# Performance work log

Hardware: AMD Instinct MI355X
Metric: run time of the kernel (lower is better)

## Reference

```python
import jax, jax.numpy as jnp
import numpy as np

EPS = 1e-8  # torch cosine_similarity norm clamp
TEMP = 1.0

def _gelu(h):
    return jax.nn.gelu(h, approximate=False)  # torch nn.GELU default (erf)

def _layernorm(h, g, b, eps=1e-5):
    mu = jnp.mean(h, axis=-1, keepdims=True)
    var = jnp.var(h, axis=-1, keepdims=True)
    return (h - mu) * jax.lax.rsqrt(var + eps) * g + b

def _encoder(h, eW1, eb1, eW2, eb2, eW3, eb3, ln_g, ln_b):
    h = _gelu(h @ eW1 + eb1)
    h = _gelu(h @ eW2 + eb2)
    h = h @ eW3 + eb3
    return _layernorm(h, ln_g, ln_b)

def _normalize(v):
    n = jnp.sqrt(jnp.sum(v * v, axis=-1, keepdims=True))
    return v / jnp.maximum(n, EPS)

def setup_inputs() -> dict:
    key = jax.random.key(0)
    ks = jax.random.split(key, 8)
    B, D, H, K = 16384, 512, 512, 11
    s = 0.02
    return {
        'x': jax.random.normal(ks[0], (B, D), jnp.float32),
        'tW1': jax.random.normal(ks[1], (K, D, H), jnp.float32) * s,
        'tb1': jnp.zeros((K, H), jnp.float32),
        'tW2': jax.random.normal(ks[2], (K, H, H), jnp.float32) * s,
        'tb2': jnp.zeros((K, H), jnp.float32),
        'tW3': jax.random.normal(ks[3], (K, H, D), jnp.float32) * s,
        'tb3': jnp.zeros((K, D), jnp.float32),
        'eW1': jax.random.normal(ks[4], (D, H), jnp.float32) * s,
        'eb1': jnp.zeros((H,), jnp.float32),
        'eW2': jax.random.normal(ks[5], (H, H), jnp.float32) * s,
        'eb2': jnp.zeros((H,), jnp.float32),
        'eW3': jax.random.normal(ks[6], (H, H), jnp.float32) * s,
        'eb3': jnp.zeros((H,), jnp.float32),
        'ln_g': jnp.ones((H,), jnp.float32),
        'ln_b': jnp.zeros((H,), jnp.float32),
    }

def reference(x, tW1, tb1, tW2, tb2, tW3, tb3, eW1, eb1, eW2, eb2, eW3, eb3, ln_g, ln_b):
    K = tW1.shape[0]
    # K learned transforms, vectorized over k: [K, B, D]
    h = _gelu(jnp.einsum('bi,kij->kbj', x, tW1) + tb1[:, None, :])
    h = _gelu(jnp.einsum('kbi,kij->kbj', h, tW2) + tb2[:, None, :])
    tx = jnp.einsum('kbi,kij->kbj', h, tW3) + tb3[:, None, :]
    # shared encoder on x and on each transformed view
    z = _encoder(x, eW1, eb1, eW2, eb2, eW3, eb3, ln_g, ln_b)      # [B, H]
    zk = _encoder(tx, eW1, eb1, eW2, eb2, eW3, eb3, ln_g, ln_b)    # [K, B, H]
    zn = _normalize(z)
    zkn = _normalize(zk)
    pos = jnp.einsum('bh,kbh->kb', zn, zkn) / TEMP                 # sim(z, z_k)
    S = jnp.einsum('lbh,kbh->lkb', zkn, zkn) / TEMP                # sim(z_l, z_k)
    diag = jnp.eye(K, dtype=bool)[:, :, None]
    Sm = jnp.where(diag, -jnp.inf, S)                              # drop l == k
    all_terms = jnp.concatenate([pos[None], Sm], axis=0)           # [K+1, K, B]
    log_den = jax.nn.logsumexp(all_terms, axis=0)                  # [K, B]
    return -jnp.sum(pos - log_den, axis=0)                         # [B]
```

## Files before the change

### kernel.cpp

```cpp
#include <hip/hip_runtime.h>
#include <hip/hip_bf16.h>
#include <cstdint>

typedef __attribute__((ext_vector_type(8))) short short8;
typedef __attribute__((ext_vector_type(4))) float f32x4;
typedef __attribute__((ext_vector_type(4))) short short4v;

__device__ __forceinline__ float b2f(short s) {
    unsigned u = ((unsigned)(unsigned short)s) << 16;
    return __builtin_bit_cast(float, u);
}
__device__ __forceinline__ short f2b(float f) {
    unsigned u = __builtin_bit_cast(unsigned, f);
    u += 0x7fff + ((u >> 16) & 1);
    return (short)(u >> 16);
}

__device__ __forceinline__ float gelu_t(float x) {
    const float c1 = 2.302184829f;
    const float c2 = 0.102947246f;
    float x2 = x * x;
    float t  = __builtin_fmaf(c2, x2, c1);
    float e  = __builtin_amdgcn_exp2f(x * t);
    return x - __fdividef(x, e + 1.0f);
}

__device__ __forceinline__ void async16(const void* g, void* l) {
    __builtin_amdgcn_global_load_lds(
        (const __attribute__((address_space(1))) unsigned int*)g,
        (__attribute__((address_space(3))) unsigned int*)l, 16, 0, 0);
}

#define VMW(N) asm volatile("s_waitcnt vmcnt(" #N ")" ::: "memory")

template<bool GELU>
__global__ __launch_bounds__(512)
void gemm_bt(const short* __restrict__ A, long sA,
             const short* __restrict__ Bt, long sB,
             const float* __restrict__ bias, long sBias,
             short* __restrict__ C, long sC) {
    const int z = blockIdx.z;
    A    += (long)z * sA;
    Bt   += (long)z * sB;
    bias += (long)z * sBias;
    C    += (long)z * sC;

    const int nwg = (int)gridDim.x;
    const int bx  = (int)blockIdx.x;
    int flat = bx;
    if ((nwg & 7) == 0) { const int q = nwg >> 3; flat = (bx & 7) * q + (bx >> 3); }
    const long arow0 = (long)(flat >> 1) * 256;
    const long brow0 = (long)(flat & 1) * 256;

    __shared__ alignas(16) short smem[2 * 32768];

    const int tid  = threadIdx.x;
    const int lane = tid & 63;
    const int w    = tid >> 6;
    const int wrow = w >> 2, wcol = w & 3;
    const int lr = lane & 15, hi = lane >> 4;

    f32x4 acc[8][4] = {};

    auto stageH = [&](int st, int sks, int sB_) {
        short* reg = smem + (st & 1) * 32768 + (sB_ ? 16384 : 0) + sks * 8192;
        const short* srcb = sB_ ? Bt : A;
        const long r0g = sB_ ? brow0 : arow0;
        const int kc = st * 64 + sks * 32;
#pragma unroll
        for (int jj = 0; jj < 2; ++jj) {
            const int R = w * 32 + jj * 16;
            const int row = R + (lane >> 2);
            const int gc = (lane & 3) ^ ((row >> 1) & 3);
            async16(srcb + (r0g + row) * 512 + kc + gc * 8, reg + R * 32);
        }
    };

    stageH(0, 0, 0); stageH(0, 0, 1);
    stageH(0, 1, 0); stageH(0, 1, 1);
    stageH(1, 0, 0); stageH(1, 0, 1);

    short8 b[4];

#pragma unroll
    for (int i = 0; i < 4; ++i) {
#pragma unroll
        for (int p = 0; p < 8; ++p) {
            const int tau = 2 * i + (p >> 2);
            const int ks  = (p >> 1) & 1;
            const int mh  = p & 1;
            const short* Ar = smem + (tau & 1) * 32768 + ks * 8192;
            const short* Br = Ar + 16384;

            if (mh == 0) {
                if (i < 3)       { VMW(8); }
                else if (p == 0) { VMW(8); }
                else if (p == 2) { VMW(8); }
                else if (p == 4) { VMW(4); }
                else             { VMW(0); }
                __builtin_amdgcn_s_barrier();
                __builtin_amdgcn_sched_barrier(0);
#pragma unroll
                for (int n = 0; n < 4; ++n) {
                    const int row = wcol * 64 + n * 16 + lr;
                    b[n] = *(const short8*)&Br[row * 32 + ((hi ^ ((row >> 1) & 3)) << 3)];
                }
            }

            short8 a[4];
#pragma unroll
            for (int j = 0; j < 4; ++j) {
                const int row = wrow * 128 + (mh * 4 + j) * 16 + lr;
                a[j] = *(const short8*)&Ar[row * 32 + ((hi ^ ((row >> 1) & 3)) << 3)];
            }

            {
                const int st  = (p < 2) ? 2 * i + 1 : (p < 6) ? 2 * i + 2 : 2 * i + 3;
                const int sks = (p < 2) ? 1 : (p < 4) ? 0 : (p < 6) ? 1 : 0;
                const int sB_ = p & 1;
                if (st < 8) stageH(st, sks, sB_);
            }

            __builtin_amdgcn_s_setprio(1);
#pragma unroll
            for (int j = 0; j < 4; ++j)
#pragma unroll
                for (int n = 0; n < 4; ++n)
                    acc[mh * 4 + j][n] = __builtin_amdgcn_mfma_f32_16x16x32_bf16(
                        a[j], b[n], acc[mh * 4 + j][n], 0, 0, 0);
            __builtin_amdgcn_s_setprio(0);

            if (mh == 1) {
                __builtin_amdgcn_sched_barrier(0);
                __builtin_amdgcn_s_barrier();
            }
        }
    }

    short* E = smem + w * (32 * 72);
    const int cl = lr, rl = hi * 4;
#pragma unroll
    for (int h = 0; h < 4; ++h) {
#pragma unroll
        for (int n = 0; n < 4; ++n) {
            const int col = (int)brow0 + wcol * 64 + n * 16 + cl;
            const float bs = bias[col];
            const int ecol = n * 16 + cl;
#pragma unroll
            for (int ml = 0; ml < 2; ++ml) {
                const int m = h * 2 + ml;
                float g0 = acc[m][n][0] + bs, g1 = acc[m][n][1] + bs;
                float g2 = acc[m][n][2] + bs, g3 = acc[m][n][3] + bs;
                if (GELU) { g0 = gelu_t(g0); g1 = gelu_t(g1); g2 = gelu_t(g2); g3 = gelu_t(g3); }
                unsigned p01, p23;
                asm("v_cvt_pk_bf16_f32 %0, %1, %2" : "=v"(p01) : "v"(g0), "v"(g1));
                asm("v_cvt_pk_bf16_f32 %0, %1, %2" : "=v"(p23) : "v"(g2), "v"(g3));
                const int r0 = ml * 16 + rl;
                E[(r0 + 0) * 72 + ecol] = (short)(p01 & 0xffff);
                E[(r0 + 1) * 72 + ecol] = (short)(p01 >> 16);
                E[(r0 + 2) * 72 + ecol] = (short)(p23 & 0xffff);
                E[(r0 + 3) * 72 + ecol] = (short)(p23 >> 16);
            }
        }
#pragma unroll
        for (int chunk = 0; chunk < 4; ++chunk) {
            const int rloc = chunk * 8 + (lane >> 3);
            const int c0   = (lane & 7) * 8;
            short8 v = *(const short8*)&E[rloc * 72 + c0];
            *(short8*)&C[(arow0 + wrow * 128 + h * 32 + rloc) * 512
                         + brow0 + wcol * 64 + c0] = v;
        }
    }
}

__global__ __launch_bounds__(256)
void transpose_conv(const float* __restrict__ src, short* __restrict__ dst) {
    __shared__ float t[32][33];
    const long moff = (long)blockIdx.z * 512 * 512;
    const float* s = src + moff;
    short* d = dst + moff;
    const int tx = threadIdx.x & 31, ty = threadIdx.x >> 5;
    const int bi = blockIdx.x, bj = blockIdx.y;
#pragma unroll
    for (int j = 0; j < 4; ++j)
        t[ty + j * 8][tx] = s[(long)(bi * 32 + ty + j * 8) * 512 + bj * 32 + tx];
    __syncthreads();
#pragma unroll
    for (int j = 0; j < 4; ++j)
        d[(long)(bj * 32 + ty + j * 8) * 512 + bi * 32 + tx] = f2b(t[tx][ty + j * 8]);
}

__global__ __launch_bounds__(256)
void conv_f32_bf16(const float* __restrict__ src, short* __restrict__ dst, long n) {
    long i = ((long)blockIdx.x * 256 + threadIdx.x) * 4;
    if (i >= n) return;
    float4 f = *(const float4*)&src[i];
    short4v o;
    o[0] = f2b(f.x); o[1] = f2b(f.y); o[2] = f2b(f.z); o[3] = f2b(f.w);
    *(short4v*)&dst[i] = o;
}

__global__ __launch_bounds__(256)
void bias_fold(const float* __restrict__ tb3, const short* __restrict__ wtE1,
               const float* __restrict__ eb1, float* __restrict__ bB) {
    const int wid = threadIdx.x >> 6, lane = threadIdx.x & 63;
    const int idx = blockIdx.x * 4 + wid;
    const int k = idx >> 9, n = idx & 511;
    short8 wv = *(const short8*)&wtE1[(long)n * 512 + lane * 8];
    const float* tb = tb3 + (long)k * 512 + lane * 8;
    float s = 0.f;
#pragma unroll
    for (int j = 0; j < 8; ++j) s += b2f(wv[j]) * tb[j];
#pragma unroll
    for (int o = 1; o < 64; o <<= 1) s += __shfl_xor(s, o, 64);
    if (lane == 0) bB[(long)(k + 1) * 512 + n] = s + eb1[n];
}

__global__ __launch_bounds__(256)
void ln_loss(const short* __restrict__ H, const float* __restrict__ g,
             const float* __restrict__ bta, float* __restrict__ out, int CH) {
    __shared__ alignas(16) short Z[4][16 * 520];
    const int wid = threadIdx.x >> 6, lane = threadIdx.x & 63;
    const long b = (long)blockIdx.x * 4 + wid;
    short* Zw = &Z[wid][0];

#pragma unroll
    for (int r = 12; r < 16; ++r)
        *(short8*)&Zw[r * 520 + lane * 8] = (short8){0, 0, 0, 0, 0, 0, 0, 0};

    for (int s = 0; s < 12; ++s) {
        short8 t = *(const short8*)&H[((long)s * CH + b) * 512 + lane * 8];
        float v[8];
        float sum = 0.f, ss = 0.f;
#pragma unroll
        for (int j = 0; j < 8; ++j) { v[j] = b2f(t[j]); sum += v[j]; ss += v[j] * v[j]; }
#pragma unroll
        for (int o = 1; o < 64; o <<= 1) { sum += __shfl_xor(sum, o, 64); ss += __shfl_xor(ss, o, 64); }
        const float mu = sum * (1.f / 512.f);
        const float rs = rsqrtf(ss * (1.f / 512.f) - mu * mu + 1e-5f);
        float y[8]; float nsq = 0.f;
#pragma unroll
        for (int j = 0; j < 8; ++j) {
            const int col = lane * 8 + j;
            y[j] = (v[j] - mu) * rs * g[col] + bta[col];
            nsq += y[j] * y[j];
        }
#pragma unroll
        for (int o = 1; o < 64; o <<= 1) nsq += __shfl_xor(nsq, o, 64);
        const float inv = 1.f / fmaxf(sqrtf(nsq), 1e-8f);
        short8 o8;
#pragma unroll
        for (int j = 0; j < 8; ++j) o8[j] = f2b(y[j] * inv);
        *(short8*)&Zw[s * 520 + lane * 8] = o8;
    }

    f32x4 acc = {0.f, 0.f, 0.f, 0.f};
    const int lr = lane & 15, hi = lane >> 4;
#pragma unroll
    for (int st = 0; st < 16; ++st) {
        short8 a = *(const short8*)&Zw[lr * 520 + st * 32 + hi * 8];
        acc = __builtin_amdgcn_mfma_f32_16x16x32_bf16(a, a, acc, 0, 0, 0);
    }
    const int col = lr;
    float lmax = -3.0e38f;
    bool valid[4];
#pragma unroll
    for (int i = 0; i < 4; ++i) {
        const int row = hi * 4 + i;
        valid[i] = (row < 12) && (row != col);
        if (valid[i]) lmax = fmaxf(lmax, acc[i]);
    }
    lmax = fmaxf(lmax, __shfl_xor(lmax, 16, 64));
    lmax = fmaxf(lmax, __shfl_xor(lmax, 32, 64));
    float esum = 0.f;
#pragma unroll
    for (int i = 0; i < 4; ++i)
        if (valid[i]) esum += __builtin_amdgcn_exp2f((acc[i] - lmax) * 1.44269504f);
    esum += __shfl_xor(esum, 16, 64);
    esum += __shfl_xor(esum, 32, 64);
    float contrib = 0.f;
    if (hi == 0 && col >= 1 && col <= 11) {
        const float logden = lmax + __builtin_amdgcn_logf(esum) * 0.6931471806f;
        contrib = acc[0] - logden;
    }
#pragma unroll
    for (int o = 1; o < 16; o <<= 1) contrib += __shfl_xor(contrib, o, 64);
    if (lane == 0) out[b] = -contrib;
}

extern "C" void kernel_launch(void* const* d_in, const int* in_sizes, int n_in,
                              void* d_out, int out_size, void* d_ws, size_t ws_size,
                              hipStream_t stream) {
    const float* x    = (const float*)d_in[0];
    const float* tW1  = (const float*)d_in[1];
    const float* tb1  = (const float*)d_in[2];
    const float* tW2  = (const float*)d_in[3];
    const float* tb2  = (const float*)d_in[4];
    const float* tW3  = (const float*)d_in[5];
    const float* tb3  = (const float*)d_in[6];
    const float* eW1  = (const float*)d_in[7];
    const float* eb1  = (const float*)d_in[8];
    const float* eW2  = (const float*)d_in[9];
    const float* eb2  = (const float*)d_in[10];
    const float* eW3  = (const float*)d_in[11];
    const float* eb3  = (const float*)d_in[12];
    const float* ln_g = (const float*)d_in[13];
    const float* ln_b = (const float*)d_in[14];

    const int  B    = in_sizes[0] / 512;
    const long WMAT = 512L * 512L;

    int  c  = 1;
    long CH = B;
    for (;;) {
        CH = (long)B / c;
        size_t need = (size_t)48 * WMAT * 2 + (512 + 12 * 512) * 4
                    + (size_t)24 * CH * 512 * 2 + 8192;
        if (need <= ws_size || CH <= 256) break;
        c <<= 1;
    }
    const long SLAB = 12L * CH * 512;

    short* wt   = (short*)d_ws;
    short* Mt   = wt + 36L * WMAT;
    float* zero512 = (float*)(Mt + 12L * WMAT);
    float* bB   = zero512 + 512;
    short* S    = (short*)(bB + 12 * 512);
    short* T    = S + SLAB;

    {
        dim3 tgK(16, 16, 11), tg1(16, 16, 1);
        transpose_conv<<<tgK, 256, 0, stream>>>(tW1, wt + 0L * WMAT);
        transpose_conv<<<tgK, 256, 0, stream>>>(tW2, wt + 11L * WMAT);
        conv_f32_bf16<<<(unsigned)((11 * WMAT / 4 + 255) / 256), 256, 0, stream>>>(
            tW3, wt + 22L * WMAT, 11 * WMAT);
        transpose_conv<<<tg1, 256, 0, stream>>>(eW1, wt + 33L * WMAT);
        transpose_conv<<<tg1, 256, 0, stream>>>(eW2, wt + 34L * WMAT);
        transpose_conv<<<tg1, 256, 0, stream>>>(eW3, wt + 35L * WMAT);

        hipMemsetAsync(zero512, 0, 512 * sizeof(float), stream);
        gemm_bt<false><<<dim3(4, 1, 11), 512, 0, stream>>>(
            wt + 33L * WMAT, 0, wt + 22L * WMAT, WMAT, zero512, 0, Mt + WMAT, WMAT);
        hipMemcpyAsync(Mt, wt + 33L * WMAT, WMAT * sizeof(short),
                       hipMemcpyDeviceToDevice, stream);
        hipMemcpyAsync(bB, eb1, 512 * sizeof(float),
                       hipMemcpyDeviceToDevice, stream);
        bias_fold<<<(11 * 512) / 4, 256, 0, stream>>>(tb3, wt + 33L * WMAT, eb1, bB);
    }

    const long SC = CH * 512;
    const dim3 gT((unsigned)(CH / 256 * 2), 1, 11);
    const dim3 gF((unsigned)(CH / 256 * 2), 1, 12);
    const dim3 gE((unsigned)(12 * CH / 256 * 2), 1, 1);

    for (int ch = 0; ch < c; ++ch) {
        conv_f32_bf16<<<(unsigned)((SC / 4 + 255) / 256), 256, 0, stream>>>(
            x + (long)ch * SC, S, SC);

        gemm_bt<true ><<<gT, 512, 0, stream>>>(S, 0,  wt + 0L * WMAT,  WMAT, tb1, 512, T + SC, SC);
        gemm_bt<true ><<<gT, 512, 0, stream>>>(T + SC, SC, wt + 11L * WMAT, WMAT, tb2, 512, S + SC, SC);
        gemm_bt<true ><<<gF, 512, 0, stream>>>(S, SC, Mt, WMAT, bB, 512, T, SC);
        gemm_bt<true ><<<gE, 512, 0, stream>>>(T, 0, wt + 34L * WMAT, 0, eb2, 0, S, 0);
        gemm_bt<false><<<gE, 512, 0, stream>>>(S, 0, wt + 35L * WMAT, 0, eb3, 0, T, 0);

        ln_loss<<<(unsigned)(CH / 4), 256, 0, stream>>>(
            T, ln_g, ln_b, (float*)d_out + (long)ch * CH, (int)CH);
    }
}
```

Before: 962.0 us.

## Fuse the per-view MLP and encoder GEMM chain into one persistent-tile kernel

Replaces the five separate batched GEMM launches with a single kernel in which each workgroup keeps a 64-row activation tile resident in LDS. It streams each layer's weights through double-buffered LDS, applies bias and GELU in place, and writes only the final encoder output. This removes the global round-trips of intermediate activations and shrinks the workspace. The risks are the much smaller M tile (64 rows against 256 before), which lowers MFMA reuse of weights and raises weight traffic. The 64KB activation tile plus weight buffers may also limit occupancy.

```diff
diff --git a/kernel.cpp b/kernel.cpp
--- a/kernel.cpp
+++ b/kernel.cpp
@@ -5,6 +5,8 @@
 typedef __attribute__((ext_vector_type(8))) short short8;
 typedef __attribute__((ext_vector_type(4))) float f32x4;
 typedef __attribute__((ext_vector_type(4))) short short4v;
+
+#define WM 262144L
 
 __device__ __forceinline__ float b2f(short s) {
     unsigned u = ((unsigned)(unsigned short)s) << 16;
@@ -32,6 +34,132 @@
 }
 
 #define VMW(N) asm volatile("s_waitcnt vmcnt(" #N ")" ::: "memory")
+
+__global__ __launch_bounds__(512)
+void mega(const short* __restrict__ xb, const short* __restrict__ wt,
+          const short* __restrict__ Mt,
+          const float* __restrict__ tb1, const float* __restrict__ tb2,
+          const float* __restrict__ bB,
+          const float* __restrict__ eb2v, const float* __restrict__ eb3v,
+          short* __restrict__ T, int CH) {
+    __shared__ alignas(16) short Ash[64 * 512];
+    __shared__ alignas(16) short Wb[2][512 * 32];
+
+    const int tid = threadIdx.x, lane = tid & 63, w = tid >> 6;
+    const int lr = lane & 15, hi = lane >> 4;
+    const int kview = blockIdx.z;
+    const long row0 = (long)blockIdx.x * 64;
+    const int L  = (kview == 0) ? 3 : 5;
+    const int NS = L * 16;
+
+#pragma unroll
+    for (int it = 0; it < 8; ++it) {
+        const int idx = it * 512 + tid;
+        const int r = idx >> 6, cch = idx & 63;
+        short8 v = *(const short8*)&xb[(row0 + r) * 512 + cch * 8];
+        *(short8*)&Ash[r * 512 + ((cch ^ (r & 15)) << 3)] = v;
+    }
+    asm volatile("s_waitcnt lgkmcnt(0)" ::: "memory");
+
+    auto wmat = [&](int l) -> const short* {
+        if (kview == 0) return (l == 0) ? Mt : (l == 1) ? wt + 34 * WM : wt + 35 * WM;
+        return (l == 0) ? wt + (long)(kview - 1) * WM
+             : (l == 1) ? wt + (long)(11 + kview - 1) * WM
+             : (l == 2) ? Mt + (long)kview * WM
+             : (l == 3) ? wt + 34 * WM : wt + 35 * WM;
+    };
+
+    auto stageW = [&](int q, int s) {
+        const short* Wsrc = wmat(s >> 4);
+        const int kc = (s & 15) * 32;
+        short* dst = &Wb[q][0];
+#pragma unroll
+        for (int i = 0; i < 4; ++i) {
+            const int R = w * 64 + i * 16;
+            const int row = R + (lane >> 2);
+            const int gc = (lane & 3) ^ ((row >> 1) & 3);
+            async16(Wsrc + (long)row * 512 + kc + gc * 8, dst + R * 32);
+        }
+    };
+
+    f32x4 acc[4][4] = {};
+    stageW(0, 0);
+    int buf = 0;
+    for (int s = 0; s < NS; ++s) {
+        if (s + 1 < NS) { stageW(buf ^ 1, s + 1); VMW(4); }
+        else            { VMW(0); }
+        __builtin_amdgcn_sched_barrier(0);
+        __builtin_amdgcn_s_barrier();
+        __builtin_amdgcn_sched_barrier(0);
+
+        const short* Wc = &Wb[buf][0];
+        short8 a[4], b[4];
+        const int ach = (s & 15) * 4 + hi;
+#pragma unroll
+        for (int n = 0; n < 4; ++n) {
+            const int nr = w * 64 + n * 16 + lr;
+            b[n] = *(const short8*)&Wc[nr * 32 + ((hi ^ ((nr >> 1) & 3)) << 3)];
+        }
+#pragma unroll
+        for (int m = 0; m < 4; ++m) {
+            const int row = m * 16 + lr;
+            a[m] = *(const short8*)&Ash[row * 512 + ((ach ^ (row & 15)) << 3)];
+        }
+        __builtin_amdgcn_s_setprio(1);
+#pragma unroll
+        for (int m = 0; m < 4; ++m)
+#pragma unroll
+            for (int n = 0; n < 4; ++n)
+                acc[m][n] = __builtin_amdgcn_mfma_f32_16x16x32_bf16(
+                    a[m], b[n], acc[m][n], 0, 0, 0);
+        __builtin_amdgcn_s_setprio(0);
+
+        __builtin_amdgcn_sched_barrier(0);
+        __builtin_amdgcn_s_barrier();
+
+        if ((s & 15) == 15) {
+            const int l = s >> 4;
+            const float* bp; bool g;
+            if (kview == 0) {
+                bp = (l == 0) ? bB : (l == 1) ? eb2v : eb3v; g = (l < 2);
+            } else {
+                bp = (l == 0) ? tb1 + (long)(kview - 1) * 512
+                   : (l == 1) ? tb2 + (long)(kview - 1) * 512
+                   : (l == 2) ? bB + (long)kview * 512
+                   : (l == 3) ? eb2v : eb3v;
+                g = (l < 4);
+            }
+#pragma unroll
+            for (int n = 0; n < 4; ++n) {
+                const int col = w * 64 + n * 16 + lr;
+                const float bv = bp[col];
+#pragma unroll
+                for (int m = 0; m < 4; ++m) {
+#pragma unroll
+                    for (int i = 0; i < 4; ++i) {
+                        const int row = m * 16 + hi * 4 + i;
+                        float v = acc[m][n][i] + bv;
+                        if (g) v = gelu_t(v);
+                        Ash[row * 512 + (((col >> 3) ^ (row & 15)) << 3) + (col & 7)] = f2b(v);
+                    }
+                    acc[m][n] = (f32x4){0.f, 0.f, 0.f, 0.f};
+                }
+            }
+            asm volatile("s_waitcnt lgkmcnt(0)" ::: "memory");
+        }
+        buf ^= 1;
+    }
+
+    __builtin_amdgcn_s_barrier();
+
+#pragma unroll
+    for (int it = 0; it < 8; ++it) {
+        const int idx = it * 512 + tid;
+        const int r = idx >> 6, cch = idx & 63;
+        short8 v = *(const short8*)&Ash[r * 512 + ((cch ^ (r & 15)) << 3)];
+        *(short8*)&T[((long)kview * CH + row0 + r) * 512 + cch * 8] = v;
+    }
+}
 
 template<bool GELU>
 __global__ __launch_bounds__(512)
@@ -81,7 +209,6 @@
     stageH(1, 0, 0); stageH(1, 0, 1);
 
     short8 b[4];
-
 #pragma unroll
     for (int i = 0; i < 4; ++i) {
 #pragma unroll
@@ -113,14 +240,12 @@
                 const int row = wrow * 128 + (mh * 4 + j) * 16 + lr;
                 a[j] = *(const short8*)&Ar[row * 32 + ((hi ^ ((row >> 1) & 3)) << 3)];
             }
-
             {
                 const int st  = (p < 2) ? 2 * i + 1 : (p < 6) ? 2 * i + 2 : 2 * i + 3;
                 const int sks = (p < 2) ? 1 : (p < 4) ? 0 : (p < 6) ? 1 : 0;
                 const int sB_ = p & 1;
                 if (st < 8) stageH(st, sks, sB_);
             }
-
             __builtin_amdgcn_s_setprio(1);
 #pragma unroll
             for (int j = 0; j < 4; ++j)
@@ -307,61 +432,53 @@
     const float* ln_g = (const float*)d_in[13];
     const float* ln_b = (const float*)d_in[14];
 
-    const int  B    = in_sizes[0] / 512;
-    const long WMAT = 512L * 512L;
+    const int  B = in_sizes[0] / 512;
 
     int  c  = 1;
     long CH = B;
     for (;;) {
         CH = (long)B / c;
-        size_t need = (size_t)48 * WMAT * 2 + (512 + 12 * 512) * 4
-                    + (size_t)24 * CH * 512 * 2 + 8192;
+        size_t need = (size_t)48 * WM * 2 + (512 + 12 * 512) * 4
+                    + (size_t)13 * CH * 512 * 2 + 8192;
         if (need <= ws_size || CH <= 256) break;
         c <<= 1;
     }
-    const long SLAB = 12L * CH * 512;
 
     short* wt   = (short*)d_ws;
-    short* Mt   = wt + 36L * WMAT;
-    float* zero512 = (float*)(Mt + 12L * WMAT);
+    short* Mt   = wt + 36L * WM;
+    float* zero512 = (float*)(Mt + 12L * WM);
     float* bB   = zero512 + 512;
-    short* S    = (short*)(bB + 12 * 512);
-    short* T    = S + SLAB;
+    short* xb   = (short*)(bB + 12 * 512);
+    short* T    = xb + CH * 512;
 
     {
         dim3 tgK(16, 16, 11), tg1(16, 16, 1);
-        transpose_conv<<<tgK, 256, 0, stream>>>(tW1, wt + 0L * WMAT);
-        transpose_conv<<<tgK, 256, 0, stream>>>(tW2, wt + 11L * WMAT);
-        conv_f32_bf16<<<(unsigned)((11 * WMAT / 4 + 255) / 256), 256, 0, stream>>>(
-            tW3, wt + 22L * WMAT, 11 * WMAT);
-        transpose_conv<<<tg1, 256, 0, stream>>>(eW1, wt + 33L * WMAT);
-        transpose_conv<<<tg1, 256, 0, stream>>>(eW2, wt + 34L * WMAT);
-        transpose_conv<<<tg1, 256, 0, stream>>>(eW3, wt + 35L * WMAT);
+        transpose_conv<<<tgK, 256, 0, stream>>>(tW1, wt + 0L * WM);
+        transpose_conv<<<tgK, 256, 0, stream>>>(tW2, wt + 11L * WM);
+        conv_f32_bf16<<<(unsigned)((11 * WM / 4 + 255) / 256), 256, 0, stream>>>(
+            tW3, wt + 22L * WM, 11 * WM);
+        transpose_conv<<<tg1, 256, 0, stream>>>(eW1, wt + 33L * WM);
+        transpose_conv<<<tg1, 256, 0, stream>>>(eW2, wt + 34L * WM);
+        transpose_conv<<<tg1, 256, 0, stream>>>(eW3, wt + 35L * WM);
 
         hipMemsetAsync(zero512, 0, 512 * sizeof(float), stream);
         gemm_bt<false><<<dim3(4, 1, 11), 512, 0, stream>>>(
-            wt + 33L * WMAT, 0, wt + 22L * WMAT, WMAT, zero512, 0, Mt + WMAT, WMAT);
-        hipMemcpyAsync(Mt, wt + 33L * WMAT, WMAT * sizeof(short),
+            wt + 33L * WM, 0, wt + 22L * WM, WM, zero512, 0, Mt + WM, WM);
+        hipMemcpyAsync(Mt, wt + 33L * WM, WM * sizeof(short),
                        hipMemcpyDeviceToDevice, stream);
         hipMemcpyAsync(bB, eb1, 512 * sizeof(float),
                        hipMemcpyDeviceToDevice, stream);
-        bias_fold<<<(11 * 512) / 4, 256, 0, stream>>>(tb3, wt + 33L * WMAT, eb1, bB);
+        bias_fold<<<(11 * 512) / 4, 256, 0, stream>>>(tb3, wt + 33L * WM, eb1, bB);
     }
 
     const long SC = CH * 512;
-    const dim3 gT((unsigned)(CH / 256 * 2), 1, 11);
-    const dim3 gF((unsigned)(CH / 256 * 2), 1, 12);
-    const dim3 gE((unsigned)(12 * CH / 256 * 2), 1, 1);
+    const dim3 gM((unsigned)(CH / 64), 1, 12);
 
     for (int ch = 0; ch < c; ++ch) {
         conv_f32_bf16<<<(unsigned)((SC / 4 + 255) / 256), 256, 0, stream>>>(
-            x + (long)ch * SC, S, SC);
-
-        gemm_bt<true ><<<gT, 512, 0, stream>>>(S, 0,  wt + 0L * WMAT,  WMAT, tb1, 512, T + SC, SC);
-        gemm_bt<true ><<<gT, 512, 0, stream>>>(T + SC, SC, wt + 11L * WMAT, WMAT, tb2, 512, S + SC, SC);
-        gemm_bt<true ><<<gF, 512, 0, stream>>>(S, SC, Mt, WMAT, bB, 512, T, SC);
-        gemm_bt<true ><<<gE, 512, 0, stream>>>(T, 0, wt + 34L * WMAT, 0, eb2, 0, S, 0);
-        gemm_bt<false><<<gE, 512, 0, stream>>>(S, 0, wt + 35L * WMAT, 0, eb3, 0, T, 0);
+            x + (long)ch * SC, xb, SC);
+
+        mega<<<gM, 512, 0, stream>>>(xb, wt, Mt, tb1, tb2, bB, eb2, eb3, T, (int)CH);
 
         ln_loss<<<(unsigned)(CH / 4), 256, 0, stream>>>(
             T, ln_g, ln_b, (float*)d_out + (long)ch * CH, (int)CH);
```

Result: slower. 1.407 ms (+46.2%).
